# Kernel optimization log

Hardware: AMD Instinct MI355X
Metric: run time of the kernel (lower is better)

Reference implementation:

```python
import jax, jax.numpy as jnp
import numpy as np

N_NODES = 100000
N_EDGES = 600000
EMB = 128
L = 5
NUM_ATOM = 119
NUM_CHIR = 3
NUM_BTYPE = 5
NUM_BDIR = 3
BN_EPS = 1e-5


def setup_inputs() -> dict:
    key = jax.random.key(0)
    ks = jax.random.split(key, 16)
    inp = {}
    inp['x'] = jax.random.randint(ks[0], (N_NODES, 2), 0, NUM_ATOM, dtype=jnp.int64 if jax.config.jax_enable_x64 else jnp.int32)
    inp['edge_index'] = jax.random.randint(ks[1], (2, N_EDGES), 0, N_NODES)
    inp['edge_attr'] = jax.random.randint(ks[2], (N_EDGES, 2), 0, NUM_BDIR)
    s = 0.05
    inp['x_emb1'] = jax.random.normal(ks[3], (NUM_ATOM, EMB), jnp.float32) * s
    inp['x_emb2'] = jax.random.normal(ks[4], (NUM_CHIR, EMB), jnp.float32) * s
    inp['edge_emb1'] = jax.random.normal(ks[5], (L, NUM_BTYPE, EMB), jnp.float32) * s
    inp['edge_emb2'] = jax.random.normal(ks[6], (L, NUM_BDIR, EMB), jnp.float32) * s
    inp['W1'] = jax.random.normal(ks[7], (L, EMB, 2 * EMB), jnp.float32) * (1.0 / np.sqrt(EMB))
    inp['b1'] = jnp.zeros((L, 2 * EMB), jnp.float32)
    inp['W2'] = jax.random.normal(ks[8], (L, 2 * EMB, EMB), jnp.float32) * (1.0 / np.sqrt(2 * EMB))
    inp['b2'] = jnp.zeros((L, EMB), jnp.float32)
    inp['eps'] = jnp.zeros((L,), jnp.float32)
    inp['gamma'] = jnp.ones((L, EMB), jnp.float32)
    inp['beta'] = jnp.zeros((L, EMB), jnp.float32)
    return inp


def reference(x, edge_index, edge_attr, x_emb1, x_emb2, edge_emb1, edge_emb2,
              W1, b1, W2, b2, eps, gamma, beta):
    N = x.shape[0]
    # node embedding: sum of two table lookups
    x0 = jnp.clip(x[:, 0], 0, x_emb1.shape[0] - 1)
    x1 = jnp.clip(x[:, 1], 0, x_emb2.shape[0] - 1)
    h = x_emb1[x0] + x_emb2[x1]  # [N, EMB]
    # add self loops (loop edge_attr = zeros -> bond type 0 / dir 0)
    loop = jnp.arange(N, dtype=edge_index.dtype)
    src = jnp.concatenate([edge_index[0], loop])  # [E+N]
    dst = jnp.concatenate([edge_index[1], loop])
    ea = jnp.concatenate([edge_attr, jnp.zeros((N, 2), dtype=edge_attr.dtype)], axis=0)
    e0 = jnp.clip(ea[:, 0], 0, edge_emb1.shape[1] - 1)
    e1 = jnp.clip(ea[:, 1], 0, edge_emb2.shape[1] - 1)
    n_layers = eps.shape[0]
    for i in range(n_layers):
        e = edge_emb1[i][e0] + edge_emb2[i][e1]              # [E+N, EMB]
        m = jax.nn.relu(h[src] + e)                           # gather + elementwise
        agg = jax.ops.segment_sum(m, dst, num_segments=N)     # scatter-add
        out = (1.0 + eps[i]) * h + agg
        # MLP: Linear -> ReLU -> Linear
        hmid = jax.nn.relu(out @ W1[i] + b1[i])
        h = hmid @ W2[i] + b2[i]
        # BatchNorm1d over nodes (batch statistics, biased variance)
        mean = jnp.mean(h, axis=0)
        var = jnp.mean((h - mean) ** 2, axis=0)
        h = (h - mean) * jax.lax.rsqrt(var + BN_EPS) * gamma[i] + beta[i]
        if i < n_layers - 1:
            h = jax.nn.relu(h)
    return h
```

## Files before the change

kernel.cpp:

```cpp
#include <hip/hip_runtime.h>

#define NN 100000
#define NPAD 100096
#define NE 600000
#define EMB 128

typedef unsigned short u16;
typedef unsigned int u32;
typedef unsigned long long u64;
typedef _Float16 half8 __attribute__((ext_vector_type(8)));
typedef float f32x4 __attribute__((ext_vector_type(4)));

__device__ __forceinline__ float4 ld4(const float* p) { return *(const float4*)p; }
__device__ __forceinline__ u32 packh2(float a, float b) {
  union { _Float16 h[2]; u32 d; } u;
  u.h[0] = (_Float16)a;
  u.h[1] = (_Float16)b;
  return u.d;
}

__global__ __launch_bounds__(256) void node_init_kernel(
    const int* __restrict__ x, const float* __restrict__ emb1,
    const float* __restrict__ emb2, _Float16* __restrict__ hb) {
  int tid = blockIdx.x * blockDim.x + threadIdx.x;
  int n = tid >> 4;
  if (n >= NN) return;
  int kc = tid & 15;
  int x0 = min(max(x[2 * n], 0), 118);
  int x1 = min(max(x[2 * n + 1], 0), 2);
  const float* p1 = emb1 + (size_t)x0 * EMB + kc * 8;
  const float* p2 = emb2 + (size_t)x1 * EMB + kc * 8;
  _Float16 o[8];
#pragma unroll
  for (int j = 0; j < 8; ++j) o[j] = (_Float16)(p1[j] + p2[j]);
  *(ulonglong2*)(hb + (size_t)n * EMB + kc * 8) = *(ulonglong2*)o;
}

__global__ __launch_bounds__(256) void hist_kernel(const int* __restrict__ ei,
                                                   int* __restrict__ deg) {
  int e = blockIdx.x * blockDim.x + threadIdx.x;
  if (e >= NE) return;
  atomicAdd(&deg[ei[NE + e]], 1);
}

__global__ __launch_bounds__(256) void scan1_kernel(const int* __restrict__ deg,
                                                    int* __restrict__ off,
                                                    int* __restrict__ bsum) {
  __shared__ int s[256];
  int t = threadIdx.x;
  int base = blockIdx.x * 1024 + t * 4;
  int v[4];
#pragma unroll
  for (int j = 0; j < 4; ++j) {
    int idx = base + j;
    v[j] = (idx < NN) ? deg[idx] : 0;
  }
  int tsum = v[0] + v[1] + v[2] + v[3];
  s[t] = tsum;
  __syncthreads();
  for (int d = 1; d < 256; d <<= 1) {
    int add = (t >= d) ? s[t - d] : 0;
    __syncthreads();
    s[t] += add;
    __syncthreads();
  }
  int run = s[t] - tsum;
#pragma unroll
  for (int j = 0; j < 4; ++j) {
    int idx = base + j;
    if (idx < NN) off[idx] = run;
    run += v[j];
  }
  if (t == 255) bsum[blockIdx.x] = s[255];
}

__global__ void scan2_kernel(int* __restrict__ bsum, int* __restrict__ off, int nb) {
  if (threadIdx.x == 0) {
    int run = 0;
    for (int b = 0; b < nb; ++b) {
      int v = bsum[b];
      bsum[b] = run;
      run += v;
    }
    off[NN] = run;
  }
}

__global__ __launch_bounds__(256) void scan3_kernel(int* __restrict__ off,
                                                    const int* __restrict__ bsum) {
  int idx = blockIdx.x * blockDim.x + threadIdx.x;
  if (idx < NN) off[idx] += bsum[idx >> 10];
}

__global__ __launch_bounds__(256) void scatter_kernel(
    const int* __restrict__ ei, const int* __restrict__ ea,
    const int* __restrict__ off, int* __restrict__ cnt, int* __restrict__ csr) {
  int e = blockIdx.x * blockDim.x + threadIdx.x;
  if (e >= NE) return;
  int d = ei[NE + e];
  int s = ei[e];
  int a0 = min(max(ea[2 * e], 0), 4);
  int a1 = min(max(ea[2 * e + 1], 0), 2);
  int code = a0 * 3 + a1;
  int r = atomicAdd(&cnt[d], 1);
  csr[off[d] + r] = s | (code << 20);
}

__global__ __launch_bounds__(256) void combo_kernel(const float* __restrict__ ee1,
                                                    const float* __restrict__ ee2,
                                                    float* __restrict__ combos) {
  int idx = blockIdx.x * blockDim.x + threadIdx.x;
  if (idx >= 5 * 15 * 128) return;
  int l = idx / (15 * 128);
  int rem = idx % (15 * 128);
  int code = rem / 128;
  int f = rem % 128;
  combos[idx] = ee1[(l * 5 + code / 3) * 128 + f] + ee2[(l * 3 + code % 3) * 128 + f];
}

__global__ __launch_bounds__(256) void prep_w_kernel(
    const float* __restrict__ W1g, const float* __restrict__ W2g,
    _Float16* __restrict__ W1f, _Float16* __restrict__ W2f) {
  int idx = blockIdx.x * blockDim.x + threadIdx.x;
  if (idx >= 40960) return;
  _Float16 o[8];
  if (idx < 20480) {
    int lane = idx & 63;
    int r = idx >> 6;
    int nt = r & 3, kt = (r >> 2) & 3, c = (r >> 4) & 3, l = r >> 6;
    int n = c * 64 + nt * 16 + (lane & 15);
    int kb = kt * 32 + (lane >> 4) * 8;
#pragma unroll
    for (int j = 0; j < 8; ++j) o[j] = (_Float16)W1g[((size_t)l * 128 + kb + j) * 256 + n];
    *(ulonglong2*)(W1f + (size_t)idx * 8) = *(ulonglong2*)o;
  } else {
    int i2 = idx - 20480;
    int lane = i2 & 63;
    int r = i2 >> 6;
    int nt = r & 7, ktl = (r >> 3) & 1, c = (r >> 4) & 3, l = r >> 6;
    int n = nt * 16 + (lane & 15);
    int kb = c * 64 + ktl * 32 + (lane >> 4) * 8;
#pragma unroll
    for (int j = 0; j < 8; ++j) o[j] = (_Float16)W2g[((size_t)l * 256 + kb + j) * 128 + n];
    *(ulonglong2*)(W2f + (size_t)i2 * 8) = *(ulonglong2*)o;
  }
}

template <bool NORM>
__global__ __launch_bounds__(256) void agg_kernel(
    const _Float16* __restrict__ hsrc, const float* __restrict__ scsh,
    const int* __restrict__ off, const int* __restrict__ csr,
    const float* __restrict__ cb, const float* __restrict__ epsp,
    _Float16* __restrict__ Af) {
  int tid = blockIdx.x * blockDim.x + threadIdx.x;
  int g = tid >> 4;
  int kc = tid & 15;
  float av[8] = {0.f, 0.f, 0.f, 0.f, 0.f, 0.f, 0.f, 0.f};
  float scv[8], shv[8];
  if (NORM) {
    float4 sa = ld4(scsh + kc * 8), sb = ld4(scsh + kc * 8 + 4);
    float4 ha = ld4(scsh + 128 + kc * 8), hbv = ld4(scsh + 128 + kc * 8 + 4);
    scv[0] = sa.x; scv[1] = sa.y; scv[2] = sa.z; scv[3] = sa.w;
    scv[4] = sb.x; scv[5] = sb.y; scv[6] = sb.z; scv[7] = sb.w;
    shv[0] = ha.x; shv[1] = ha.y; shv[2] = ha.z; shv[3] = ha.w;
    shv[4] = hbv.x; shv[5] = hbv.y; shv[6] = hbv.z; shv[7] = hbv.w;
  }
  if (g < NN) {
    const float eps1 = 1.0f + *epsp;
    ulonglong2 hraw = *(const ulonglong2*)(hsrc + (size_t)g * EMB + kc * 8);
    _Float16* hr = (_Float16*)&hraw;
    float4 ca = ld4(cb + kc * 8), cbv = ld4(cb + kc * 8 + 4);
    float cs[8] = {ca.x, ca.y, ca.z, ca.w, cbv.x, cbv.y, cbv.z, cbv.w};
#pragma unroll
    for (int j = 0; j < 8; ++j) {
      float hv = (float)hr[j];
      if (NORM) hv = fmaxf(hv * scv[j] + shv[j], 0.f);
      av[j] = eps1 * hv + fmaxf(hv + cs[j], 0.f);
    }
    int s0 = off[g], s1 = off[g + 1];
    int e = s0;
    for (; e + 3 < s1; e += 4) {
      int p0 = csr[e], p1 = csr[e + 1], p2 = csr[e + 2], p3 = csr[e + 3];
      ulonglong2 r0 = *(const ulonglong2*)(hsrc + (size_t)(p0 & 0xFFFFF) * EMB + kc * 8);
      ulonglong2 r1 = *(const ulonglong2*)(hsrc + (size_t)(p1 & 0xFFFFF) * EMB + kc * 8);
      ulonglong2 r2 = *(const ulonglong2*)(hsrc + (size_t)(p2 & 0xFFFFF) * EMB + kc * 8);
      ulonglong2 r3 = *(const ulonglong2*)(hsrc + (size_t)(p3 & 0xFFFFF) * EMB + kc * 8);
      ulonglong2 rr[4] = {r0, r1, r2, r3};
      int pp[4] = {p0, p1, p2, p3};
#pragma unroll
      for (int u = 0; u < 4; ++u) {
        const float* cp = cb + (size_t)(pp[u] >> 20) * EMB + kc * 8;
        float4 c0 = ld4(cp), c1 = ld4(cp + 4);
        float cc[8] = {c0.x, c0.y, c0.z, c0.w, c1.x, c1.y, c1.z, c1.w};
        _Float16* sp = (_Float16*)&rr[u];
#pragma unroll
        for (int j = 0; j < 8; ++j) {
          float v = (float)sp[j];
          if (NORM) v = fmaxf(v * scv[j] + shv[j], 0.f);
          av[j] += fmaxf(v + cc[j], 0.f);
        }
      }
    }
    for (; e < s1; ++e) {
      int p0 = csr[e];
      ulonglong2 r0 = *(const ulonglong2*)(hsrc + (size_t)(p0 & 0xFFFFF) * EMB + kc * 8);
      const float* cp = cb + (size_t)(p0 >> 20) * EMB + kc * 8;
      float4 c0 = ld4(cp), c1 = ld4(cp + 4);
      float cc[8] = {c0.x, c0.y, c0.z, c0.w, c1.x, c1.y, c1.z, c1.w};
      _Float16* sp = (_Float16*)&r0;
#pragma unroll
      for (int j = 0; j < 8; ++j) {
        float v = (float)sp[j];
        if (NORM) v = fmaxf(v * scv[j] + shv[j], 0.f);
        av[j] += fmaxf(v + cc[j], 0.f);
      }
    }
  }
  _Float16 o[8];
#pragma unroll
  for (int j = 0; j < 8; ++j) o[j] = (_Float16)av[j];
  *(ulonglong2*)(Af + (size_t)g * EMB + kc * 8) = *(ulonglong2*)o;
}

__global__ __launch_bounds__(512, 2) void mlp_kernel(
    const _Float16* __restrict__ Af, const _Float16* __restrict__ W1f,
    const _Float16* __restrict__ W2f,
    const float* __restrict__ b1g, const float* __restrict__ b2g,
    _Float16* __restrict__ hpre, float* __restrict__ slots) {
  extern __shared__ __align__(16) _Float16 Ws[];
  _Float16* W1s = Ws;
  _Float16* W2s = Ws + 32768;

  const int t = threadIdx.x;
  const int w = t >> 6;
  const int lane = t & 63;
  const int q = lane >> 4, l15 = lane & 15;
  const int gw = blockIdx.x * 8 + w;
  const int n0 = blockIdx.x * 256 + w * 32;
  float* sums = slots + (size_t)(gw & 31) * 256;

  half8 nh[2][4];
#pragma unroll
  for (int ntile = 0; ntile < 2; ++ntile)
#pragma unroll
    for (int kt = 0; kt < 4; ++kt)
      nh[ntile][kt] =
          *(const half8*)(Af + (size_t)(n0 + ntile * 16 + l15) * EMB + kt * 32 + q * 8);

  {
    ulonglong2* d1 = (ulonglong2*)W1s;
    ulonglong2* d2 = (ulonglong2*)W2s;
    const ulonglong2* g1 = (const ulonglong2*)W1f;
    const ulonglong2* g2 = (const ulonglong2*)W2f;
#pragma unroll
    for (int j = 0; j < 8; ++j) d1[t + j * 512] = g1[t + j * 512];
#pragma unroll
    for (int j = 0; j < 8; ++j) d2[t + j * 512] = g2[t + j * 512];
  }
  __syncthreads();

  f32x4 oacc[2][8];
#pragma unroll
  for (int ntile = 0; ntile < 2; ++ntile)
#pragma unroll
    for (int a = 0; a < 8; ++a) oacc[ntile][a] = (f32x4){0.f, 0.f, 0.f, 0.f};

  const int srcA = ((q & 1) * 2) * 16 + l15;
  const int srcB = srcA + 16;
  const bool sel = (q >> 1) != 0;

  for (int c = 0; c < 4; ++c) {
    f32x4 hacc[2][4];
#pragma unroll
    for (int ntile = 0; ntile < 2; ++ntile)
#pragma unroll
      for (int a = 0; a < 4; ++a) hacc[ntile][a] = (f32x4){0.f, 0.f, 0.f, 0.f};
#pragma unroll
    for (int kt = 0; kt < 4; ++kt) {
      half8 wh[4];
#pragma unroll
      for (int colt = 0; colt < 4; ++colt)
        wh[colt] = *(const half8*)&W1s[(c * 16 + kt * 4 + colt) * 512 + lane * 8];
#pragma unroll
      for (int colt = 0; colt < 4; ++colt) {
        hacc[0][colt] =
            __builtin_amdgcn_mfma_f32_16x16x32_f16(wh[colt], nh[0][kt], hacc[0][colt], 0, 0, 0);
        hacc[1][colt] =
            __builtin_amdgcn_mfma_f32_16x16x32_f16(wh[colt], nh[1][kt], hacc[1][colt], 0, 0, 0);
      }
    }

    u32 P01[2][4], P23[2][4];
#pragma unroll
    for (int colt = 0; colt < 4; ++colt) {
      float4 b1v = ld4(b1g + c * 64 + colt * 16 + q * 4);
#pragma unroll
      for (int ntile = 0; ntile < 2; ++ntile) {
        float v0 = fmaxf(hacc[ntile][colt][0] + b1v.x, 0.f);
        float v1 = fmaxf(hacc[ntile][colt][1] + b1v.y, 0.f);
        float v2 = fmaxf(hacc[ntile][colt][2] + b1v.z, 0.f);
        float v3 = fmaxf(hacc[ntile][colt][3] + b1v.w, 0.f);
        P01[ntile][colt] = packh2(v0, v1);
        P23[ntile][colt] = packh2(v2, v3);
      }
    }

#pragma unroll
    for (int ktl = 0; ktl < 2; ++ktl) {
      half8 bh[2];
#pragma unroll
      for (int ntile = 0; ntile < 2; ++ntile) {
        union { u32 d[4]; half8 s; } uh;
        int c0 = 2 * ktl, c1 = 2 * ktl + 1;
        u32 a0, a1;
        a0 = (u32)__shfl((int)P01[ntile][c0], srcA);
        a1 = (u32)__shfl((int)P01[ntile][c1], srcA);
        uh.d[0] = sel ? a1 : a0;
        a0 = (u32)__shfl((int)P23[ntile][c0], srcA);
        a1 = (u32)__shfl((int)P23[ntile][c1], srcA);
        uh.d[1] = sel ? a1 : a0;
        a0 = (u32)__shfl((int)P01[ntile][c0], srcB);
        a1 = (u32)__shfl((int)P01[ntile][c1], srcB);
        uh.d[2] = sel ? a1 : a0;
        a0 = (u32)__shfl((int)P23[ntile][c0], srcB);
        a1 = (u32)__shfl((int)P23[ntile][c1], srcB);
        uh.d[3] = sel ? a1 : a0;
        bh[ntile] = uh.s;
      }
#pragma unroll
      for (int nt = 0; nt < 8; ++nt) {
        half8 wh = *(const half8*)&W2s[(c * 16 + ktl * 8 + nt) * 512 + lane * 8];
        oacc[0][nt] = __builtin_amdgcn_mfma_f32_16x16x32_f16(wh, bh[0], oacc[0][nt], 0, 0, 0);
        oacc[1][nt] = __builtin_amdgcn_mfma_f32_16x16x32_f16(wh, bh[1], oacc[1][nt], 0, 0, 0);
      }
    }
  }

#pragma unroll
  for (int nt = 0; nt < 8; ++nt) {
    int ocb = nt * 16 + q * 4;
    float4 b2v = ld4(b2g + ocb);
    f32x4 s = (f32x4){0.f, 0.f, 0.f, 0.f};
    f32x4 s2 = (f32x4){0.f, 0.f, 0.f, 0.f};
#pragma unroll
    for (int ntile = 0; ntile < 2; ++ntile) {
      int node = n0 + ntile * 16 + l15;
      if (node < NN) {
        float v0 = oacc[ntile][nt][0] + b2v.x;
        float v1 = oacc[ntile][nt][1] + b2v.y;
        float v2 = oacc[ntile][nt][2] + b2v.z;
        float v3 = oacc[ntile][nt][3] + b2v.w;
        u64 pk = (u64)packh2(v0, v1) | ((u64)packh2(v2, v3) << 32);
        *(u64*)(hpre + (size_t)node * EMB + ocb) = pk;
        s[0] += v0; s[1] += v1; s[2] += v2; s[3] += v3;
        s2[0] += v0 * v0; s2[1] += v1 * v1; s2[2] += v2 * v2; s2[3] += v3 * v3;
      }
    }
#pragma unroll
    for (int d = 1; d < 16; d <<= 1) {
#pragma unroll
      for (int r = 0; r < 4; ++r) {
        s[r] += __shfl_xor(s[r], d);
        s2[r] += __shfl_xor(s2[r], d);
      }
    }
    if (l15 == 0) {
#pragma unroll
      for (int r = 0; r < 4; ++r) {
        atomicAdd(&sums[ocb + r], s[r]);
        atomicAdd(&sums[128 + ocb + r], s2[r]);
      }
    }
  }
}

__global__ void stats_kernel(const float* __restrict__ slots,
                             const float* __restrict__ gamma,
                             const float* __restrict__ beta,
                             float* __restrict__ scsh) {
  int f = threadIdx.x;
  float s = 0.f, s2 = 0.f;
#pragma unroll 8
  for (int k = 0; k < 32; ++k) {
    s += slots[k * 256 + f];
    s2 += slots[k * 256 + 128 + f];
  }
  float mean = s * (1.0f / NN);
  float var = s2 * (1.0f / NN) - mean * mean;
  float sc = gamma[f] * rsqrtf(var + 1e-5f);
  scsh[f] = sc;
  scsh[128 + f] = beta[f] - mean * sc;
}

__global__ __launch_bounds__(256) void out_kernel(
    const _Float16* __restrict__ hpre, const float* __restrict__ scsh,
    float* __restrict__ out) {
  int tid = blockIdx.x * blockDim.x + threadIdx.x;
  int n = tid >> 4;
  if (n >= NN) return;
  int kc = tid & 15;
  ulonglong2 raw = *(const ulonglong2*)(hpre + (size_t)n * EMB + kc * 8);
  _Float16* hr = (_Float16*)&raw;
  float4 sa = ld4(scsh + kc * 8), sb = ld4(scsh + kc * 8 + 4);
  float4 ha = ld4(scsh + 128 + kc * 8), hbv = ld4(scsh + 128 + kc * 8 + 4);
  float scv[8] = {sa.x, sa.y, sa.z, sa.w, sb.x, sb.y, sb.z, sb.w};
  float shv[8] = {ha.x, ha.y, ha.z, ha.w, hbv.x, hbv.y, hbv.z, hbv.w};
  float v[8];
#pragma unroll
  for (int j = 0; j < 8; ++j) v[j] = (float)hr[j] * scv[j] + shv[j];
  float* d = out + (size_t)n * EMB + kc * 8;
  *(float4*)d = make_float4(v[0], v[1], v[2], v[3]);
  *(float4*)(d + 4) = make_float4(v[4], v[5], v[6], v[7]);
}

extern "C" void kernel_launch(void* const* d_in, const int* in_sizes, int n_in,
                              void* d_out, int out_size, void* d_ws, size_t ws_size,
                              hipStream_t stream) {
  const int* x = (const int*)d_in[0];
  const int* ei = (const int*)d_in[1];
  const int* ea = (const int*)d_in[2];
  const float* x_emb1 = (const float*)d_in[3];
  const float* x_emb2 = (const float*)d_in[4];
  const float* ee1 = (const float*)d_in[5];
  const float* ee2 = (const float*)d_in[6];
  const float* W1 = (const float*)d_in[7];
  const float* b1 = (const float*)d_in[8];
  const float* W2 = (const float*)d_in[9];
  const float* b2 = (const float*)d_in[10];
  const float* eps = (const float*)d_in[11];
  const float* gamma = (const float*)d_in[12];
  const float* beta = (const float*)d_in[13];
  float* out = (float*)d_out;

  static int _attr_once = []() {
    hipFuncSetAttribute((const void*)mlp_kernel,
                        hipFuncAttributeMaxDynamicSharedMemorySize, 131072);
    return 0;
  }();
  (void)_attr_once;

  float* slots = (float*)d_ws;
  float* scsh = slots + 5 * 32 * 256;
  float* combos = scsh + 5 * 256;
  _Float16* hpre = (_Float16*)(combos + 9600);
  _Float16* Af = hpre + (size_t)NN * EMB;
  _Float16* hb = Af + (size_t)NPAD * EMB;
  _Float16* W1f = hb + (size_t)NN * EMB;
  _Float16* W2f = W1f + 5 * 32768;
  int* deg = (int*)(W2f + 5 * 32768);
  int* off = deg + NN;
  int* csr = off + NN + 1;
  int* bsum = csr + NE;

  const int NB_SCAN = (NN + 1023) / 1024;

  hipMemsetAsync(deg, 0, NN * sizeof(int), stream);
  hipMemsetAsync(slots, 0, 5 * 32 * 256 * sizeof(float), stream);
  hist_kernel<<<(NE + 255) / 256, 256, 0, stream>>>(ei, deg);
  scan1_kernel<<<NB_SCAN, 256, 0, stream>>>(deg, off, bsum);
  scan2_kernel<<<1, 64, 0, stream>>>(bsum, off, NB_SCAN);
  scan3_kernel<<<(NN + 255) / 256, 256, 0, stream>>>(off, bsum);
  hipMemsetAsync(deg, 0, NN * sizeof(int), stream);
  scatter_kernel<<<(NE + 255) / 256, 256, 0, stream>>>(ei, ea, off, deg, csr);
  combo_kernel<<<(5 * 15 * 128 + 255) / 256, 256, 0, stream>>>(ee1, ee2, combos);
  prep_w_kernel<<<160, 256, 0, stream>>>(W1, W2, W1f, W2f);
  node_init_kernel<<<NN * 16 / 256 + 1, 256, 0, stream>>>(x, x_emb1, x_emb2, hb);

  const int MLP_GRID = NPAD / 256;
  for (int i = 0; i < 5; ++i) {
    if (i == 0)
      agg_kernel<false><<<NPAD * 16 / 256, 256, 0, stream>>>(
          hb, nullptr, off, csr, combos + (size_t)i * 15 * EMB, eps + i, Af);
    else
      agg_kernel<true><<<NPAD * 16 / 256, 256, 0, stream>>>(
          hpre, scsh + (size_t)(i - 1) * 256, off, csr,
          combos + (size_t)i * 15 * EMB, eps + i, Af);
    mlp_kernel<<<MLP_GRID, 512, 131072, stream>>>(
        Af, W1f + (size_t)i * 32768, W2f + (size_t)i * 32768,
        b1 + (size_t)i * 256, b2 + (size_t)i * 128, hpre,
        slots + (size_t)i * 32 * 256);
    stats_kernel<<<1, 128, 0, stream>>>(slots + (size_t)i * 32 * 256,
                                        gamma + (size_t)i * EMB,
                                        beta + (size_t)i * EMB,
                                        scsh + (size_t)i * 256);
  }
  out_kernel<<<NN * 16 / 256 + 1, 256, 0, stream>>>(hpre, scsh + 4 * 256, out);
}
```

Measured before the change: 673.0 us.

## Switch MLP kernel to 32x32x16 MFMA with permlane32 swap for hidden relayout

Rewrites the fused MLP kernel to use 32x32x16 f16 MFMA tiles (one 32-node tile per wave) instead of pairs of 16x16x32 tiles. The hidden-layer relayout between the two GEMMs now uses v_permlane32_swap instead of many cross-lane shuffles and selects. The weight prepacking layout is changed to match. Larger MFMAs cut LDS weight reads and instruction count, but the BN statistics reduction now needs a 5-step shuffle over 16 registers each for sum and sum-of-squares, and register pressure rises.

```diff
diff --git a/kernel.cpp b/kernel.cpp
--- a/kernel.cpp
+++ b/kernel.cpp
@@ -10,6 +10,7 @@
 typedef unsigned long long u64;
 typedef _Float16 half8 __attribute__((ext_vector_type(8)));
 typedef float f32x4 __attribute__((ext_vector_type(4)));
+typedef float f32x16 __attribute__((ext_vector_type(16)));
 
 __device__ __forceinline__ float4 ld4(const float* p) { return *(const float4*)p; }
 __device__ __forceinline__ u32 packh2(float a, float b) {
@@ -17,6 +18,9 @@
   u.h[0] = (_Float16)a;
   u.h[1] = (_Float16)b;
   return u.d;
+}
+__device__ __forceinline__ void pl32swap(u32& a, u32& b) {
+  asm volatile("v_permlane32_swap_b32 %0, %1" : "+v"(a), "+v"(b));
 }
 
 __global__ __launch_bounds__(256) void node_init_kernel(
@@ -127,21 +131,23 @@
   if (idx < 20480) {
     int lane = idx & 63;
     int r = idx >> 6;
-    int nt = r & 3, kt = (r >> 2) & 3, c = (r >> 4) & 3, l = r >> 6;
-    int n = c * 64 + nt * 16 + (lane & 15);
-    int kb = kt * 32 + (lane >> 4) * 8;
-#pragma unroll
-    for (int j = 0; j < 8; ++j) o[j] = (_Float16)W1g[((size_t)l * 128 + kb + j) * 256 + n];
+    int ks = r & 7, mb = (r >> 3) & 7, l = r >> 6;
+    int hi = lane >> 5, l31 = lane & 31;
+    int kb = ks * 16 + hi * 8;
+    int mid = mb * 32 + l31;
+#pragma unroll
+    for (int j = 0; j < 8; ++j) o[j] = (_Float16)W1g[((size_t)l * 128 + kb + j) * 256 + mid];
     *(ulonglong2*)(W1f + (size_t)idx * 8) = *(ulonglong2*)o;
   } else {
     int i2 = idx - 20480;
     int lane = i2 & 63;
     int r = i2 >> 6;
-    int nt = r & 7, ktl = (r >> 3) & 1, c = (r >> 4) & 3, l = r >> 6;
-    int n = nt * 16 + (lane & 15);
-    int kb = c * 64 + ktl * 32 + (lane >> 4) * 8;
-#pragma unroll
-    for (int j = 0; j < 8; ++j) o[j] = (_Float16)W2g[((size_t)l * 256 + kb + j) * 128 + n];
+    int ks2 = r & 15, ob = (r >> 4) & 3, l = r >> 6;
+    int hi = lane >> 5, l31 = lane & 31;
+    int kb = ks2 * 16 + hi * 8;
+    int oc = ob * 32 + l31;
+#pragma unroll
+    for (int j = 0; j < 8; ++j) o[j] = (_Float16)W2g[((size_t)l * 256 + kb + j) * 128 + oc];
     *(ulonglong2*)(W2f + (size_t)i2 * 8) = *(ulonglong2*)o;
   }
 }
@@ -234,142 +240,130 @@
   const int t = threadIdx.x;
   const int w = t >> 6;
   const int lane = t & 63;
-  const int q = lane >> 4, l15 = lane & 15;
+  const int hi = lane >> 5, l31 = lane & 31;
   const int gw = blockIdx.x * 8 + w;
   const int n0 = blockIdx.x * 256 + w * 32;
+  const int node = n0 + l31;
   float* sums = slots + (size_t)(gw & 31) * 256;
 
-  half8 nh[2][4];
-#pragma unroll
-  for (int ntile = 0; ntile < 2; ++ntile)
-#pragma unroll
-    for (int kt = 0; kt < 4; ++kt)
-      nh[ntile][kt] =
-          *(const half8*)(Af + (size_t)(n0 + ntile * 16 + l15) * EMB + kt * 32 + q * 8);
+  half8 nh[8];
+#pragma unroll
+  for (int ks = 0; ks < 8; ++ks)
+    nh[ks] = *(const half8*)(Af + (size_t)node * EMB + ks * 16 + hi * 8);
 
   {
-    ulonglong2* d1 = (ulonglong2*)W1s;
-    ulonglong2* d2 = (ulonglong2*)W2s;
+    ulonglong2* d1 = (ulonglong2*)Ws;
     const ulonglong2* g1 = (const ulonglong2*)W1f;
     const ulonglong2* g2 = (const ulonglong2*)W2f;
 #pragma unroll
     for (int j = 0; j < 8; ++j) d1[t + j * 512] = g1[t + j * 512];
 #pragma unroll
-    for (int j = 0; j < 8; ++j) d2[t + j * 512] = g2[t + j * 512];
+    for (int j = 0; j < 8; ++j) d1[4096 + t + j * 512] = g2[t + j * 512];
   }
   __syncthreads();
 
-  f32x4 oacc[2][8];
-#pragma unroll
-  for (int ntile = 0; ntile < 2; ++ntile)
-#pragma unroll
-    for (int a = 0; a < 8; ++a) oacc[ntile][a] = (f32x4){0.f, 0.f, 0.f, 0.f};
-
-  const int srcA = ((q & 1) * 2) * 16 + l15;
-  const int srcB = srcA + 16;
-  const bool sel = (q >> 1) != 0;
-
+  f32x16 oacc[4];
+#pragma unroll
+  for (int ob = 0; ob < 4; ++ob)
+#pragma unroll
+    for (int r = 0; r < 16; ++r) oacc[ob][r] = 0.f;
+
+#pragma unroll
   for (int c = 0; c < 4; ++c) {
-    f32x4 hacc[2][4];
-#pragma unroll
-    for (int ntile = 0; ntile < 2; ++ntile)
-#pragma unroll
-      for (int a = 0; a < 4; ++a) hacc[ntile][a] = (f32x4){0.f, 0.f, 0.f, 0.f};
-#pragma unroll
-    for (int kt = 0; kt < 4; ++kt) {
-      half8 wh[4];
-#pragma unroll
-      for (int colt = 0; colt < 4; ++colt)
-        wh[colt] = *(const half8*)&W1s[(c * 16 + kt * 4 + colt) * 512 + lane * 8];
-#pragma unroll
-      for (int colt = 0; colt < 4; ++colt) {
-        hacc[0][colt] =
-            __builtin_amdgcn_mfma_f32_16x16x32_f16(wh[colt], nh[0][kt], hacc[0][colt], 0, 0, 0);
-        hacc[1][colt] =
-            __builtin_amdgcn_mfma_f32_16x16x32_f16(wh[colt], nh[1][kt], hacc[1][colt], 0, 0, 0);
-      }
-    }
-
-    u32 P01[2][4], P23[2][4];
-#pragma unroll
-    for (int colt = 0; colt < 4; ++colt) {
-      float4 b1v = ld4(b1g + c * 64 + colt * 16 + q * 4);
-#pragma unroll
-      for (int ntile = 0; ntile < 2; ++ntile) {
-        float v0 = fmaxf(hacc[ntile][colt][0] + b1v.x, 0.f);
-        float v1 = fmaxf(hacc[ntile][colt][1] + b1v.y, 0.f);
-        float v2 = fmaxf(hacc[ntile][colt][2] + b1v.z, 0.f);
-        float v3 = fmaxf(hacc[ntile][colt][3] + b1v.w, 0.f);
-        P01[ntile][colt] = packh2(v0, v1);
-        P23[ntile][colt] = packh2(v2, v3);
-      }
-    }
-
-#pragma unroll
-    for (int ktl = 0; ktl < 2; ++ktl) {
-      half8 bh[2];
-#pragma unroll
-      for (int ntile = 0; ntile < 2; ++ntile) {
-        union { u32 d[4]; half8 s; } uh;
-        int c0 = 2 * ktl, c1 = 2 * ktl + 1;
-        u32 a0, a1;
-        a0 = (u32)__shfl((int)P01[ntile][c0], srcA);
-        a1 = (u32)__shfl((int)P01[ntile][c1], srcA);
-        uh.d[0] = sel ? a1 : a0;
-        a0 = (u32)__shfl((int)P23[ntile][c0], srcA);
-        a1 = (u32)__shfl((int)P23[ntile][c1], srcA);
-        uh.d[1] = sel ? a1 : a0;
-        a0 = (u32)__shfl((int)P01[ntile][c0], srcB);
-        a1 = (u32)__shfl((int)P01[ntile][c1], srcB);
-        uh.d[2] = sel ? a1 : a0;
-        a0 = (u32)__shfl((int)P23[ntile][c0], srcB);
-        a1 = (u32)__shfl((int)P23[ntile][c1], srcB);
-        uh.d[3] = sel ? a1 : a0;
-        bh[ntile] = uh.s;
-      }
-#pragma unroll
-      for (int nt = 0; nt < 8; ++nt) {
-        half8 wh = *(const half8*)&W2s[(c * 16 + ktl * 8 + nt) * 512 + lane * 8];
-        oacc[0][nt] = __builtin_amdgcn_mfma_f32_16x16x32_f16(wh, bh[0], oacc[0][nt], 0, 0, 0);
-        oacc[1][nt] = __builtin_amdgcn_mfma_f32_16x16x32_f16(wh, bh[1], oacc[1][nt], 0, 0, 0);
-      }
-    }
-  }
-
-#pragma unroll
-  for (int nt = 0; nt < 8; ++nt) {
-    int ocb = nt * 16 + q * 4;
-    float4 b2v = ld4(b2g + ocb);
-    f32x4 s = (f32x4){0.f, 0.f, 0.f, 0.f};
-    f32x4 s2 = (f32x4){0.f, 0.f, 0.f, 0.f};
-#pragma unroll
-    for (int ntile = 0; ntile < 2; ++ntile) {
-      int node = n0 + ntile * 16 + l15;
-      if (node < NN) {
-        float v0 = oacc[ntile][nt][0] + b2v.x;
-        float v1 = oacc[ntile][nt][1] + b2v.y;
-        float v2 = oacc[ntile][nt][2] + b2v.z;
-        float v3 = oacc[ntile][nt][3] + b2v.w;
-        u64 pk = (u64)packh2(v0, v1) | ((u64)packh2(v2, v3) << 32);
-        *(u64*)(hpre + (size_t)node * EMB + ocb) = pk;
-        s[0] += v0; s[1] += v1; s[2] += v2; s[3] += v3;
-        s2[0] += v0 * v0; s2[1] += v1 * v1; s2[2] += v2 * v2; s2[3] += v3 * v3;
-      }
-    }
-#pragma unroll
-    for (int d = 1; d < 16; d <<= 1) {
-#pragma unroll
-      for (int r = 0; r < 4; ++r) {
-        s[r] += __shfl_xor(s[r], d);
-        s2[r] += __shfl_xor(s2[r], d);
-      }
-    }
-    if (l15 == 0) {
-#pragma unroll
-      for (int r = 0; r < 4; ++r) {
-        atomicAdd(&sums[ocb + r], s[r]);
-        atomicAdd(&sums[128 + ocb + r], s2[r]);
-      }
+    f32x16 hacc[2];
+#pragma unroll
+    for (int b = 0; b < 2; ++b)
+#pragma unroll
+      for (int r = 0; r < 16; ++r) hacc[b][r] = 0.f;
+#pragma unroll
+    for (int ks = 0; ks < 8; ++ks) {
+      half8 w0 = *(const half8*)&W1s[((2 * c + 0) * 8 + ks) * 512 + lane * 8];
+      half8 w1 = *(const half8*)&W1s[((2 * c + 1) * 8 + ks) * 512 + lane * 8];
+      hacc[0] = __builtin_amdgcn_mfma_f32_32x32x16_f16(w0, nh[ks], hacc[0], 0, 0, 0);
+      hacc[1] = __builtin_amdgcn_mfma_f32_32x32x16_f16(w1, nh[ks], hacc[1], 0, 0, 0);
+    }
+
+    half8 bf[2][2];
+#pragma unroll
+    for (int b = 0; b < 2; ++b) {
+      u32 pk[8];
+      const int mbase = (2 * c + b) * 32;
+#pragma unroll
+      for (int m = 0; m < 4; ++m) {
+        float4 b1v = ld4(b1g + mbase + m * 8 + 4 * hi);
+        float v0 = fmaxf(hacc[b][4 * m + 0] + b1v.x, 0.f);
+        float v1 = fmaxf(hacc[b][4 * m + 1] + b1v.y, 0.f);
+        float v2 = fmaxf(hacc[b][4 * m + 2] + b1v.z, 0.f);
+        float v3 = fmaxf(hacc[b][4 * m + 3] + b1v.w, 0.f);
+        pk[2 * m + 0] = packh2(v0, v1);
+        pk[2 * m + 1] = packh2(v2, v3);
+      }
+      pl32swap(pk[0], pk[2]);
+      pl32swap(pk[1], pk[3]);
+      pl32swap(pk[4], pk[6]);
+      pl32swap(pk[5], pk[7]);
+      union { u32 d[4]; half8 h; } lo, hb2;
+      lo.d[0] = pk[0]; lo.d[1] = pk[1]; lo.d[2] = pk[2]; lo.d[3] = pk[3];
+      hb2.d[0] = pk[4]; hb2.d[1] = pk[5]; hb2.d[2] = pk[6]; hb2.d[3] = pk[7];
+      bf[b][0] = lo.h;
+      bf[b][1] = hb2.h;
+    }
+
+#pragma unroll
+    for (int ob = 0; ob < 4; ++ob) {
+#pragma unroll
+      for (int kk = 0; kk < 4; ++kk) {
+        half8 wA = *(const half8*)&W2s[(ob * 16 + c * 4 + kk) * 512 + lane * 8];
+        oacc[ob] =
+            __builtin_amdgcn_mfma_f32_32x32x16_f16(wA, bf[kk >> 1][kk & 1], oacc[ob], 0, 0, 0);
+      }
+    }
+  }
+
+  const bool ok = node < NN;
+#pragma unroll
+  for (int ob = 0; ob < 4; ++ob) {
+    float sv[16];
+#pragma unroll
+    for (int m = 0; m < 4; ++m) {
+      float4 b2v = ld4(b2g + ob * 32 + m * 8 + 4 * hi);
+      sv[4 * m + 0] = oacc[ob][4 * m + 0] + b2v.x;
+      sv[4 * m + 1] = oacc[ob][4 * m + 1] + b2v.y;
+      sv[4 * m + 2] = oacc[ob][4 * m + 2] + b2v.z;
+      sv[4 * m + 3] = oacc[ob][4 * m + 3] + b2v.w;
+    }
+    if (ok) {
+#pragma unroll
+      for (int m = 0; m < 4; ++m) {
+        u64 pkv = (u64)packh2(sv[4 * m + 0], sv[4 * m + 1]) |
+                  ((u64)packh2(sv[4 * m + 2], sv[4 * m + 3]) << 32);
+        *(u64*)(hpre + (size_t)node * EMB + ob * 32 + m * 8 + 4 * hi) = pkv;
+      }
+    }
+    float s1a[16], s2a[16];
+#pragma unroll
+    for (int r = 0; r < 16; ++r) {
+      float v = ok ? sv[r] : 0.f;
+      s1a[r] = v;
+      s2a[r] = v * v;
+    }
+#pragma unroll
+    for (int d = 1; d < 32; d <<= 1) {
+#pragma unroll
+      for (int r = 0; r < 16; ++r) {
+        s1a[r] += __shfl_xor(s1a[r], d);
+        s2a[r] += __shfl_xor(s2a[r], d);
+      }
+    }
+    if (l31 == 0) {
+#pragma unroll
+      for (int m = 0; m < 4; ++m)
+#pragma unroll
+        for (int r = 0; r < 4; ++r) {
+          int oc = ob * 32 + m * 8 + 4 * hi + r;
+          atomicAdd(&sums[oc], s1a[4 * m + r]);
+          atomicAdd(&sums[128 + oc], s2a[4 * m + r]);
+        }
     }
   }
 }
```

Result: slower. 774.8 us (+15.1%).

## Fuse neighbor aggregation into persistent MLP kernel with atomic tile queue

Applied to the files above, without the earlier changes.

Merges the gather/aggregation kernel into the MFMA MLP kernel so each wave aggregates 32 nodes directly into MFMA operand registers, removing the Af intermediate round-trip through global memory. The fused kernel is persistent (256 blocks) and pulls 32-node tiles from an atomic counter, loading weights into LDS once per block. Edge-combo embeddings are stored as fp16, and h ping-pongs between two buffers because the kernel reads neighbors while writing outputs. In exchange, the gather now runs at much lower occupancy (512 threads, 128KB LDS), with each lane handling 4x more features per node, so latency hiding for the random gathers may be worse.

```diff
diff --git a/kernel.cpp b/kernel.cpp
--- a/kernel.cpp
+++ b/kernel.cpp
@@ -2,6 +2,7 @@
 
 #define NN 100000
 #define NPAD 100096
+#define NTILES 3128
 #define NE 600000
 #define EMB 128
 
@@ -12,6 +13,11 @@
 typedef float f32x4 __attribute__((ext_vector_type(4)));
 
 __device__ __forceinline__ float4 ld4(const float* p) { return *(const float4*)p; }
+__device__ __forceinline__ void ld8(const float* p, float* o) {
+  float4 a = ld4(p), b = ld4(p + 4);
+  o[0] = a.x; o[1] = a.y; o[2] = a.z; o[3] = a.w;
+  o[4] = b.x; o[5] = b.y; o[6] = b.z; o[7] = b.w;
+}
 __device__ __forceinline__ u32 packh2(float a, float b) {
   union { _Float16 h[2]; u32 d; } u;
   u.h[0] = (_Float16)a;
@@ -108,14 +114,14 @@
 
 __global__ __launch_bounds__(256) void combo_kernel(const float* __restrict__ ee1,
                                                     const float* __restrict__ ee2,
-                                                    float* __restrict__ combos) {
+                                                    _Float16* __restrict__ cbh) {
   int idx = blockIdx.x * blockDim.x + threadIdx.x;
   if (idx >= 5 * 15 * 128) return;
   int l = idx / (15 * 128);
   int rem = idx % (15 * 128);
   int code = rem / 128;
   int f = rem % 128;
-  combos[idx] = ee1[(l * 5 + code / 3) * 128 + f] + ee2[(l * 3 + code % 3) * 128 + f];
+  cbh[idx] = (_Float16)(ee1[(l * 5 + code / 3) * 128 + f] + ee2[(l * 3 + code % 3) * 128 + f]);
 }
 
 __global__ __launch_bounds__(256) void prep_w_kernel(
@@ -147,228 +153,242 @@
 }
 
 template <bool NORM>
-__global__ __launch_bounds__(256) void agg_kernel(
+__global__ __launch_bounds__(512, 2) void fused_kernel(
     const _Float16* __restrict__ hsrc, const float* __restrict__ scsh,
     const int* __restrict__ off, const int* __restrict__ csr,
-    const float* __restrict__ cb, const float* __restrict__ epsp,
-    _Float16* __restrict__ Af) {
-  int tid = blockIdx.x * blockDim.x + threadIdx.x;
-  int g = tid >> 4;
-  int kc = tid & 15;
-  float av[8] = {0.f, 0.f, 0.f, 0.f, 0.f, 0.f, 0.f, 0.f};
-  float scv[8], shv[8];
-  if (NORM) {
-    float4 sa = ld4(scsh + kc * 8), sb = ld4(scsh + kc * 8 + 4);
-    float4 ha = ld4(scsh + 128 + kc * 8), hbv = ld4(scsh + 128 + kc * 8 + 4);
-    scv[0] = sa.x; scv[1] = sa.y; scv[2] = sa.z; scv[3] = sa.w;
-    scv[4] = sb.x; scv[5] = sb.y; scv[6] = sb.z; scv[7] = sb.w;
-    shv[0] = ha.x; shv[1] = ha.y; shv[2] = ha.z; shv[3] = ha.w;
-    shv[4] = hbv.x; shv[5] = hbv.y; shv[6] = hbv.z; shv[7] = hbv.w;
-  }
-  if (g < NN) {
-    const float eps1 = 1.0f + *epsp;
-    ulonglong2 hraw = *(const ulonglong2*)(hsrc + (size_t)g * EMB + kc * 8);
-    _Float16* hr = (_Float16*)&hraw;
-    float4 ca = ld4(cb + kc * 8), cbv = ld4(cb + kc * 8 + 4);
-    float cs[8] = {ca.x, ca.y, ca.z, ca.w, cbv.x, cbv.y, cbv.z, cbv.w};
-#pragma unroll
-    for (int j = 0; j < 8; ++j) {
-      float hv = (float)hr[j];
-      if (NORM) hv = fmaxf(hv * scv[j] + shv[j], 0.f);
-      av[j] = eps1 * hv + fmaxf(hv + cs[j], 0.f);
-    }
-    int s0 = off[g], s1 = off[g + 1];
-    int e = s0;
-    for (; e + 3 < s1; e += 4) {
-      int p0 = csr[e], p1 = csr[e + 1], p2 = csr[e + 2], p3 = csr[e + 3];
-      ulonglong2 r0 = *(const ulonglong2*)(hsrc + (size_t)(p0 & 0xFFFFF) * EMB + kc * 8);
-      ulonglong2 r1 = *(const ulonglong2*)(hsrc + (size_t)(p1 & 0xFFFFF) * EMB + kc * 8);
-      ulonglong2 r2 = *(const ulonglong2*)(hsrc + (size_t)(p2 & 0xFFFFF) * EMB + kc * 8);
-      ulonglong2 r3 = *(const ulonglong2*)(hsrc + (size_t)(p3 & 0xFFFFF) * EMB + kc * 8);
-      ulonglong2 rr[4] = {r0, r1, r2, r3};
-      int pp[4] = {p0, p1, p2, p3};
-#pragma unroll
-      for (int u = 0; u < 4; ++u) {
-        const float* cp = cb + (size_t)(pp[u] >> 20) * EMB + kc * 8;
-        float4 c0 = ld4(cp), c1 = ld4(cp + 4);
-        float cc[8] = {c0.x, c0.y, c0.z, c0.w, c1.x, c1.y, c1.z, c1.w};
-        _Float16* sp = (_Float16*)&rr[u];
-#pragma unroll
-        for (int j = 0; j < 8; ++j) {
-          float v = (float)sp[j];
-          if (NORM) v = fmaxf(v * scv[j] + shv[j], 0.f);
-          av[j] += fmaxf(v + cc[j], 0.f);
-        }
-      }
-    }
-    for (; e < s1; ++e) {
-      int p0 = csr[e];
-      ulonglong2 r0 = *(const ulonglong2*)(hsrc + (size_t)(p0 & 0xFFFFF) * EMB + kc * 8);
-      const float* cp = cb + (size_t)(p0 >> 20) * EMB + kc * 8;
-      float4 c0 = ld4(cp), c1 = ld4(cp + 4);
-      float cc[8] = {c0.x, c0.y, c0.z, c0.w, c1.x, c1.y, c1.z, c1.w};
-      _Float16* sp = (_Float16*)&r0;
-#pragma unroll
-      for (int j = 0; j < 8; ++j) {
-        float v = (float)sp[j];
-        if (NORM) v = fmaxf(v * scv[j] + shv[j], 0.f);
-        av[j] += fmaxf(v + cc[j], 0.f);
-      }
-    }
-  }
-  _Float16 o[8];
-#pragma unroll
-  for (int j = 0; j < 8; ++j) o[j] = (_Float16)av[j];
-  *(ulonglong2*)(Af + (size_t)g * EMB + kc * 8) = *(ulonglong2*)o;
-}
-
-__global__ __launch_bounds__(512, 2) void mlp_kernel(
-    const _Float16* __restrict__ Af, const _Float16* __restrict__ W1f,
-    const _Float16* __restrict__ W2f,
+    const _Float16* __restrict__ cbh, const float* __restrict__ epsp,
+    const _Float16* __restrict__ W1f, const _Float16* __restrict__ W2f,
     const float* __restrict__ b1g, const float* __restrict__ b2g,
-    _Float16* __restrict__ hpre, float* __restrict__ slots) {
+    _Float16* __restrict__ hout, float* __restrict__ slots, int* __restrict__ ctr) {
   extern __shared__ __align__(16) _Float16 Ws[];
   _Float16* W1s = Ws;
   _Float16* W2s = Ws + 32768;
 
   const int t = threadIdx.x;
-  const int w = t >> 6;
   const int lane = t & 63;
   const int q = lane >> 4, l15 = lane & 15;
-  const int gw = blockIdx.x * 8 + w;
-  const int n0 = blockIdx.x * 256 + w * 32;
-  float* sums = slots + (size_t)(gw & 31) * 256;
-
-  half8 nh[2][4];
-#pragma unroll
-  for (int ntile = 0; ntile < 2; ++ntile)
-#pragma unroll
-    for (int kt = 0; kt < 4; ++kt)
-      nh[ntile][kt] =
-          *(const half8*)(Af + (size_t)(n0 + ntile * 16 + l15) * EMB + kt * 32 + q * 8);
 
   {
-    ulonglong2* d1 = (ulonglong2*)W1s;
-    ulonglong2* d2 = (ulonglong2*)W2s;
+    ulonglong2* d1 = (ulonglong2*)Ws;
     const ulonglong2* g1 = (const ulonglong2*)W1f;
     const ulonglong2* g2 = (const ulonglong2*)W2f;
 #pragma unroll
     for (int j = 0; j < 8; ++j) d1[t + j * 512] = g1[t + j * 512];
 #pragma unroll
-    for (int j = 0; j < 8; ++j) d2[t + j * 512] = g2[t + j * 512];
+    for (int j = 0; j < 8; ++j) d1[4096 + t + j * 512] = g2[t + j * 512];
   }
   __syncthreads();
 
-  f32x4 oacc[2][8];
-#pragma unroll
-  for (int ntile = 0; ntile < 2; ++ntile)
-#pragma unroll
-    for (int a = 0; a < 8; ++a) oacc[ntile][a] = (f32x4){0.f, 0.f, 0.f, 0.f};
-
+  const float eps1 = 1.0f + *epsp;
   const int srcA = ((q & 1) * 2) * 16 + l15;
   const int srcB = srcA + 16;
   const bool sel = (q >> 1) != 0;
 
-  for (int c = 0; c < 4; ++c) {
-    f32x4 hacc[2][4];
+  while (true) {
+    int tile = 0;
+    if (lane == 0) tile = atomicAdd(ctr, 1);
+    tile = __shfl(tile, 0);
+    if (tile >= NTILES) break;
+    const int n0 = tile * 32;
+
+    float scv[4][8], shv[4][8];
+    if (NORM) {
+#pragma unroll
+      for (int kt = 0; kt < 4; ++kt) {
+        ld8(scsh + kt * 32 + q * 8, scv[kt]);
+        ld8(scsh + 128 + kt * 32 + q * 8, shv[kt]);
+      }
+    }
+    half8 c0h[4];
+#pragma unroll
+    for (int kt = 0; kt < 4; ++kt) c0h[kt] = *(const half8*)(cbh + kt * 32 + q * 8);
+
+    half8 nh[2][4];
+#pragma unroll
+    for (int ntile = 0; ntile < 2; ++ntile) {
+      const int node = n0 + ntile * 16 + l15;
+      float av[4][8];
+#pragma unroll
+      for (int kt = 0; kt < 4; ++kt)
+#pragma unroll
+        for (int j = 0; j < 8; ++j) av[kt][j] = 0.f;
+      if (node < NN) {
+        half8 sr[4];
+#pragma unroll
+        for (int kt = 0; kt < 4; ++kt)
+          sr[kt] = *(const half8*)(hsrc + (size_t)node * EMB + kt * 32 + q * 8);
+#pragma unroll
+        for (int kt = 0; kt < 4; ++kt)
+#pragma unroll
+          for (int j = 0; j < 8; ++j) {
+            float hv = (float)sr[kt][j];
+            if (NORM) hv = fmaxf(hv * scv[kt][j] + shv[kt][j], 0.f);
+            av[kt][j] = eps1 * hv + fmaxf(hv + (float)c0h[kt][j], 0.f);
+          }
+        const int e1 = off[node + 1];
+        int e = off[node];
+        for (; e + 1 < e1; e += 2) {
+          int p0 = csr[e], p1 = csr[e + 1];
+          const _Float16* r0p = hsrc + (size_t)(p0 & 0xFFFFF) * EMB;
+          const _Float16* r1p = hsrc + (size_t)(p1 & 0xFFFFF) * EMB;
+          const _Float16* c0p = cbh + (size_t)(p0 >> 20) * EMB;
+          const _Float16* c1p = cbh + (size_t)(p1 >> 20) * EMB;
+          half8 r0[4], r1[4], cc0[4], cc1[4];
+#pragma unroll
+          for (int kt = 0; kt < 4; ++kt) {
+            r0[kt] = *(const half8*)(r0p + kt * 32 + q * 8);
+            r1[kt] = *(const half8*)(r1p + kt * 32 + q * 8);
+            cc0[kt] = *(const half8*)(c0p + kt * 32 + q * 8);
+            cc1[kt] = *(const half8*)(c1p + kt * 32 + q * 8);
+          }
+#pragma unroll
+          for (int kt = 0; kt < 4; ++kt)
+#pragma unroll
+            for (int j = 0; j < 8; ++j) {
+              float v0 = (float)r0[kt][j], v1 = (float)r1[kt][j];
+              if (NORM) {
+                v0 = fmaxf(v0 * scv[kt][j] + shv[kt][j], 0.f);
+                v1 = fmaxf(v1 * scv[kt][j] + shv[kt][j], 0.f);
+              }
+              av[kt][j] += fmaxf(v0 + (float)cc0[kt][j], 0.f);
+              av[kt][j] += fmaxf(v1 + (float)cc1[kt][j], 0.f);
+            }
+        }
+        for (; e < e1; ++e) {
+          int p0 = csr[e];
+          const _Float16* r0p = hsrc + (size_t)(p0 & 0xFFFFF) * EMB;
+          const _Float16* c0p = cbh + (size_t)(p0 >> 20) * EMB;
+          half8 r0[4], cc0[4];
+#pragma unroll
+          for (int kt = 0; kt < 4; ++kt) {
+            r0[kt] = *(const half8*)(r0p + kt * 32 + q * 8);
+            cc0[kt] = *(const half8*)(c0p + kt * 32 + q * 8);
+          }
+#pragma unroll
+          for (int kt = 0; kt < 4; ++kt)
+#pragma unroll
+            for (int j = 0; j < 8; ++j) {
+              float v0 = (float)r0[kt][j];
+              if (NORM) v0 = fmaxf(v0 * scv[kt][j] + shv[kt][j], 0.f);
+              av[kt][j] += fmaxf(v0 + (float)cc0[kt][j], 0.f);
+            }
+        }
+      }
+#pragma unroll
+      for (int kt = 0; kt < 4; ++kt) {
+        half8 o;
+#pragma unroll
+        for (int j = 0; j < 8; ++j) o[j] = (_Float16)av[kt][j];
+        nh[ntile][kt] = o;
+      }
+    }
+
+    f32x4 oacc[2][8];
 #pragma unroll
     for (int ntile = 0; ntile < 2; ++ntile)
 #pragma unroll
-      for (int a = 0; a < 4; ++a) hacc[ntile][a] = (f32x4){0.f, 0.f, 0.f, 0.f};
-#pragma unroll
-    for (int kt = 0; kt < 4; ++kt) {
-      half8 wh[4];
-#pragma unroll
-      for (int colt = 0; colt < 4; ++colt)
-        wh[colt] = *(const half8*)&W1s[(c * 16 + kt * 4 + colt) * 512 + lane * 8];
+      for (int a = 0; a < 8; ++a) oacc[ntile][a] = (f32x4){0.f, 0.f, 0.f, 0.f};
+
+#pragma unroll
+    for (int c = 0; c < 4; ++c) {
+      f32x4 hacc[2][4];
+#pragma unroll
+      for (int ntile = 0; ntile < 2; ++ntile)
+#pragma unroll
+        for (int a = 0; a < 4; ++a) hacc[ntile][a] = (f32x4){0.f, 0.f, 0.f, 0.f};
+#pragma unroll
+      for (int kt = 0; kt < 4; ++kt) {
+#pragma unroll
+        for (int colt = 0; colt < 4; ++colt) {
+          half8 wh = *(const half8*)&W1s[(c * 16 + kt * 4 + colt) * 512 + lane * 8];
+          hacc[0][colt] =
+              __builtin_amdgcn_mfma_f32_16x16x32_f16(wh, nh[0][kt], hacc[0][colt], 0, 0, 0);
+          hacc[1][colt] =
+              __builtin_amdgcn_mfma_f32_16x16x32_f16(wh, nh[1][kt], hacc[1][colt], 0, 0, 0);
+        }
+      }
+
+      u32 P01[2][4], P23[2][4];
 #pragma unroll
       for (int colt = 0; colt < 4; ++colt) {
-        hacc[0][colt] =
-            __builtin_amdgcn_mfma_f32_16x16x32_f16(wh[colt], nh[0][kt], hacc[0][colt], 0, 0, 0);
-        hacc[1][colt] =
-            __builtin_amdgcn_mfma_f32_16x16x32_f16(wh[colt], nh[1][kt], hacc[1][colt], 0, 0, 0);
+        float4 b1v = ld4(b1g + c * 64 + colt * 16 + q * 4);
+#pragma unroll
+        for (int ntile = 0; ntile < 2; ++ntile) {
+          float v0 = fmaxf(hacc[ntile][colt][0] + b1v.x, 0.f);
+          float v1 = fmaxf(hacc[ntile][colt][1] + b1v.y, 0.f);
+          float v2 = fmaxf(hacc[ntile][colt][2] + b1v.z, 0.f);
+          float v3 = fmaxf(hacc[ntile][colt][3] + b1v.w, 0.f);
+          P01[ntile][colt] = packh2(v0, v1);
+          P23[ntile][colt] = packh2(v2, v3);
+        }
+      }
+
+#pragma unroll
+      for (int ktl = 0; ktl < 2; ++ktl) {
+        half8 bh[2];
+#pragma unroll
+        for (int ntile = 0; ntile < 2; ++ntile) {
+          union { u32 d[4]; half8 s; } uh;
+          int c0 = 2 * ktl, c1 = 2 * ktl + 1;
+          u32 a0, a1;
+          a0 = (u32)__shfl((int)P01[ntile][c0], srcA);
+          a1 = (u32)__shfl((int)P01[ntile][c1], srcA);
+          uh.d[0] = sel ? a1 : a0;
+          a0 = (u32)__shfl((int)P23[ntile][c0], srcA);
+          a1 = (u32)__shfl((int)P23[ntile][c1], srcA);
+          uh.d[1] = sel ? a1 : a0;
+          a0 = (u32)__shfl((int)P01[ntile][c0], srcB);
+          a1 = (u32)__shfl((int)P01[ntile][c1], srcB);
+          uh.d[2] = sel ? a1 : a0;
+          a0 = (u32)__shfl((int)P23[ntile][c0], srcB);
+          a1 = (u32)__shfl((int)P23[ntile][c1], srcB);
+          uh.d[3] = sel ? a1 : a0;
+          bh[ntile] = uh.s;
+        }
+#pragma unroll
+        for (int nt = 0; nt < 8; ++nt) {
+          half8 wh = *(const half8*)&W2s[(c * 16 + ktl * 8 + nt) * 512 + lane * 8];
+          oacc[0][nt] = __builtin_amdgcn_mfma_f32_16x16x32_f16(wh, bh[0], oacc[0][nt], 0, 0, 0);
+          oacc[1][nt] = __builtin_amdgcn_mfma_f32_16x16x32_f16(wh, bh[1], oacc[1][nt], 0, 0, 0);
+        }
       }
     }
 
-    u32 P01[2][4], P23[2][4];
-#pragma unroll
-    for (int colt = 0; colt < 4; ++colt) {
-      float4 b1v = ld4(b1g + c * 64 + colt * 16 + q * 4);
+    float* sums = slots + (size_t)(tile & 31) * 256;
+#pragma unroll
+    for (int nt = 0; nt < 8; ++nt) {
+      int ocb = nt * 16 + q * 4;
+      float4 b2v = ld4(b2g + ocb);
+      f32x4 s = (f32x4){0.f, 0.f, 0.f, 0.f};
+      f32x4 s2 = (f32x4){0.f, 0.f, 0.f, 0.f};
 #pragma unroll
       for (int ntile = 0; ntile < 2; ++ntile) {
-        float v0 = fmaxf(hacc[ntile][colt][0] + b1v.x, 0.f);
-        float v1 = fmaxf(hacc[ntile][colt][1] + b1v.y, 0.f);
-        float v2 = fmaxf(hacc[ntile][colt][2] + b1v.z, 0.f);
-        float v3 = fmaxf(hacc[ntile][colt][3] + b1v.w, 0.f);
-        P01[ntile][colt] = packh2(v0, v1);
-        P23[ntile][colt] = packh2(v2, v3);
-      }
-    }
-
-#pragma unroll
-    for (int ktl = 0; ktl < 2; ++ktl) {
-      half8 bh[2];
-#pragma unroll
-      for (int ntile = 0; ntile < 2; ++ntile) {
-        union { u32 d[4]; half8 s; } uh;
-        int c0 = 2 * ktl, c1 = 2 * ktl + 1;
-        u32 a0, a1;
-        a0 = (u32)__shfl((int)P01[ntile][c0], srcA);
-        a1 = (u32)__shfl((int)P01[ntile][c1], srcA);
-        uh.d[0] = sel ? a1 : a0;
-        a0 = (u32)__shfl((int)P23[ntile][c0], srcA);
-        a1 = (u32)__shfl((int)P23[ntile][c1], srcA);
-        uh.d[1] = sel ? a1 : a0;
-        a0 = (u32)__shfl((int)P01[ntile][c0], srcB);
-        a1 = (u32)__shfl((int)P01[ntile][c1], srcB);
-        uh.d[2] = sel ? a1 : a0;
-        a0 = (u32)__shfl((int)P23[ntile][c0], srcB);
-        a1 = (u32)__shfl((int)P23[ntile][c1], srcB);
-        uh.d[3] = sel ? a1 : a0;
-        bh[ntile] = uh.s;
-      }
-#pragma unroll
-      for (int nt = 0; nt < 8; ++nt) {
-        half8 wh = *(const half8*)&W2s[(c * 16 + ktl * 8 + nt) * 512 + lane * 8];
-        oacc[0][nt] = __builtin_amdgcn_mfma_f32_16x16x32_f16(wh, bh[0], oacc[0][nt], 0, 0, 0);
-        oacc[1][nt] = __builtin_amdgcn_mfma_f32_16x16x32_f16(wh, bh[1], oacc[1][nt], 0, 0, 0);
-      }
-    }
-  }
-
-#pragma unroll
-  for (int nt = 0; nt < 8; ++nt) {
-    int ocb = nt * 16 + q * 4;
-    float4 b2v = ld4(b2g + ocb);
-    f32x4 s = (f32x4){0.f, 0.f, 0.f, 0.f};
-    f32x4 s2 = (f32x4){0.f, 0.f, 0.f, 0.f};
-#pragma unroll
-    for (int ntile = 0; ntile < 2; ++ntile) {
-      int node = n0 + ntile * 16 + l15;
-      if (node < NN) {
-        float v0 = oacc[ntile][nt][0] + b2v.x;
-        float v1 = oacc[ntile][nt][1] + b2v.y;
-        float v2 = oacc[ntile][nt][2] + b2v.z;
-        float v3 = oacc[ntile][nt][3] + b2v.w;
-        u64 pk = (u64)packh2(v0, v1) | ((u64)packh2(v2, v3) << 32);
-        *(u64*)(hpre + (size_t)node * EMB + ocb) = pk;
-        s[0] += v0; s[1] += v1; s[2] += v2; s[3] += v3;
-        s2[0] += v0 * v0; s2[1] += v1 * v1; s2[2] += v2 * v2; s2[3] += v3 * v3;
-      }
-    }
-#pragma unroll
-    for (int d = 1; d < 16; d <<= 1) {
-#pragma unroll
-      for (int r = 0; r < 4; ++r) {
-        s[r] += __shfl_xor(s[r], d);
-        s2[r] += __shfl_xor(s2[r], d);
-      }
-    }
-    if (l15 == 0) {
-#pragma unroll
-      for (int r = 0; r < 4; ++r) {
-        atomicAdd(&sums[ocb + r], s[r]);
-        atomicAdd(&sums[128 + ocb + r], s2[r]);
+        int node = n0 + ntile * 16 + l15;
+        if (node < NN) {
+          float v0 = oacc[ntile][nt][0] + b2v.x;
+          float v1 = oacc[ntile][nt][1] + b2v.y;
+          float v2 = oacc[ntile][nt][2] + b2v.z;
+          float v3 = oacc[ntile][nt][3] + b2v.w;
+          u64 pk = (u64)packh2(v0, v1) | ((u64)packh2(v2, v3) << 32);
+          *(u64*)(hout + (size_t)node * EMB + ocb) = pk;
+          s[0] += v0; s[1] += v1; s[2] += v2; s[3] += v3;
+          s2[0] += v0 * v0; s2[1] += v1 * v1; s2[2] += v2 * v2; s2[3] += v3 * v3;
+        }
+      }
+#pragma unroll
+      for (int d = 1; d < 16; d <<= 1) {
+#pragma unroll
+        for (int r = 0; r < 4; ++r) {
+          s[r] += __shfl_xor(s[r], d);
+          s2[r] += __shfl_xor(s2[r], d);
+        }
+      }
+      if (l15 == 0) {
+#pragma unroll
+        for (int r = 0; r < 4; ++r) {
+          atomicAdd(&sums[ocb + r], s[r]);
+          atomicAdd(&sums[128 + ocb + r], s2[r]);
+        }
       }
     }
   }
@@ -433,7 +453,9 @@
   float* out = (float*)d_out;
 
   static int _attr_once = []() {
-    hipFuncSetAttribute((const void*)mlp_kernel,
+    hipFuncSetAttribute((const void*)fused_kernel<false>,
+                        hipFuncAttributeMaxDynamicSharedMemorySize, 131072);
+    hipFuncSetAttribute((const void*)fused_kernel<true>,
                         hipFuncAttributeMaxDynamicSharedMemorySize, 131072);
     return 0;
   }();
@@ -441,48 +463,48 @@
 
   float* slots = (float*)d_ws;
   float* scsh = slots + 5 * 32 * 256;
-  float* combos = scsh + 5 * 256;
-  _Float16* hpre = (_Float16*)(combos + 9600);
-  _Float16* Af = hpre + (size_t)NN * EMB;
-  _Float16* hb = Af + (size_t)NPAD * EMB;
+  _Float16* hp0 = (_Float16*)(scsh + 5 * 256);
+  _Float16* hp1 = hp0 + (size_t)NN * EMB;
+  _Float16* hb = hp1 + (size_t)NN * EMB;
   _Float16* W1f = hb + (size_t)NN * EMB;
   _Float16* W2f = W1f + 5 * 32768;
-  int* deg = (int*)(W2f + 5 * 32768);
+  _Float16* cbh = W2f + 5 * 32768;
+  int* deg = (int*)(cbh + 5 * 15 * 128);
   int* off = deg + NN;
   int* csr = off + NN + 1;
   int* bsum = csr + NE;
+  int* ctrs = bsum + 128;
 
   const int NB_SCAN = (NN + 1023) / 1024;
 
   hipMemsetAsync(deg, 0, NN * sizeof(int), stream);
   hipMemsetAsync(slots, 0, 5 * 32 * 256 * sizeof(float), stream);
+  hipMemsetAsync(ctrs, 0, 8 * sizeof(int), stream);
   hist_kernel<<<(NE + 255) / 256, 256, 0, stream>>>(ei, deg);
   scan1_kernel<<<NB_SCAN, 256, 0, stream>>>(deg, off, bsum);
   scan2_kernel<<<1, 64, 0, stream>>>(bsum, off, NB_SCAN);
   scan3_kernel<<<(NN + 255) / 256, 256, 0, stream>>>(off, bsum);
   hipMemsetAsync(deg, 0, NN * sizeof(int), stream);
   scatter_kernel<<<(NE + 255) / 256, 256, 0, stream>>>(ei, ea, off, deg, csr);
-  combo_kernel<<<(5 * 15 * 128 + 255) / 256, 256, 0, stream>>>(ee1, ee2, combos);
+  combo_kernel<<<(5 * 15 * 128 + 255) / 256, 256, 0, stream>>>(ee1, ee2, cbh);
   prep_w_kernel<<<160, 256, 0, stream>>>(W1, W2, W1f, W2f);
   node_init_kernel<<<NN * 16 / 256 + 1, 256, 0, stream>>>(x, x_emb1, x_emb2, hb);
 
-  const int MLP_GRID = NPAD / 256;
   for (int i = 0; i < 5; ++i) {
+    _Float16* wr = (i & 1) ? hp1 : hp0;
     if (i == 0)
-      agg_kernel<false><<<NPAD * 16 / 256, 256, 0, stream>>>(
-          hb, nullptr, off, csr, combos + (size_t)i * 15 * EMB, eps + i, Af);
+      fused_kernel<false><<<256, 512, 131072, stream>>>(
+          hb, nullptr, off, csr, cbh, eps, W1f, W2f, b1, b2, wr, slots, ctrs);
     else
-      agg_kernel<true><<<NPAD * 16 / 256, 256, 0, stream>>>(
-          hpre, scsh + (size_t)(i - 1) * 256, off, csr,
-          combos + (size_t)i * 15 * EMB, eps + i, Af);
-    mlp_kernel<<<MLP_GRID, 512, 131072, stream>>>(
-        Af, W1f + (size_t)i * 32768, W2f + (size_t)i * 32768,
-        b1 + (size_t)i * 256, b2 + (size_t)i * 128, hpre,
-        slots + (size_t)i * 32 * 256);
+      fused_kernel<true><<<256, 512, 131072, stream>>>(
+          (i & 1) ? hp0 : hp1, scsh + (size_t)(i - 1) * 256, off, csr,
+          cbh + (size_t)i * 15 * EMB, eps + i, W1f + (size_t)i * 32768,
+          W2f + (size_t)i * 32768, b1 + (size_t)i * 256, b2 + (size_t)i * 128, wr,
+          slots + (size_t)i * 32 * 256, ctrs + i);
     stats_kernel<<<1, 128, 0, stream>>>(slots + (size_t)i * 32 * 256,
                                         gamma + (size_t)i * EMB,
                                         beta + (size_t)i * EMB,
                                         scsh + (size_t)i * 256);
   }
-  out_kernel<<<NN * 16 / 256 + 1, 256, 0, stream>>>(hpre, scsh + 4 * 256, out);
-}
+  out_kernel<<<NN * 16 / 256 + 1, 256, 0, stream>>>(hp0, scsh + 4 * 256, out);
+}
```

Measured after the change: 884.9 us. 31.5% more time.
